# Optimization experiments

Measured on AMD Instinct MI355X. Metric: run time of the kernel, lower is better.

Reference implementation:

```python
import jax, jax.numpy as jnp
import numpy as np

DECAY = 0.99
EPSILON = 1e-05
CODEBOOK_SIZE = 1024
DIM = 128


def setup_inputs() -> dict:
    key = jax.random.key(0)
    k1, k2, k3, k4 = jax.random.split(key, 4)
    x = jax.random.normal(k1, (8, 8192, DIM), dtype=jnp.float32)
    embed = jax.random.normal(k2, (CODEBOOK_SIZE, DIM), dtype=jnp.float32)
    cluster_size = jax.random.uniform(k3, (CODEBOOK_SIZE,), dtype=jnp.float32)
    embed_avg = jax.random.normal(k4, (CODEBOOK_SIZE, DIM), dtype=jnp.float32)
    return {"x": x, "embed": embed, "cluster_size": cluster_size, "embed_avg": embed_avg}


def reference(x, embed, cluster_size, embed_avg):
    shape = x.shape
    flat = x.reshape(-1, shape[-1])  # [N, dim]

    # quantize: negative squared euclidean distance, argmax == nearest code
    dist = -(jnp.sum(flat * flat, axis=1, keepdims=True)
             - 2.0 * flat @ embed.T
             + jnp.sum(embed * embed, axis=1)[None, :])  # [N, K]
    embed_ind = jnp.argmax(dist, axis=-1)  # [N]

    quantize = embed[embed_ind].reshape(shape)            # dequantize
    embed_ind_out = embed_ind.reshape(shape[:-1])

    # training-time EMA updates (one-hot expressed as segment_sum)
    batch_cluster_size = jax.ops.segment_sum(
        jnp.ones_like(embed_ind, dtype=flat.dtype), embed_ind,
        num_segments=CODEBOOK_SIZE)                       # == one_hot.sum(0)
    new_cluster_size = cluster_size * DECAY + (1.0 - DECAY) * batch_cluster_size

    embed_sum = jax.ops.segment_sum(flat, embed_ind,
                                    num_segments=CODEBOOK_SIZE)  # == (x.T @ one_hot).T
    new_embed_avg = embed_avg * DECAY + (1.0 - DECAY) * embed_sum

    total = new_cluster_size.sum()
    smoothed = (new_cluster_size + EPSILON) / (total + CODEBOOK_SIZE * EPSILON)
    smoothed_counts = smoothed * total
    new_embed = new_embed_avg / smoothed_counts[:, None]

    return quantize, embed_ind_out, new_cluster_size, new_embed_avg, new_embed
```

## Files before the change

kernel.cpp:

```cpp
#include <hip/hip_runtime.h>
#include <math.h>

#define DIM 128
#define KCODES 1024
#define NROWS 65536

typedef short bf16x8 __attribute__((ext_vector_type(8)));
typedef float f32x4 __attribute__((ext_vector_type(4)));

#define WS_COUNTS 0
#define WS_ESUM   1024
#define WS_IOFF   132096
#define WS_TOTAL  133120
#define WS_ENORM2 133124
#define WS_EBF    134148
#define WS_WIN    461828
#define WS_SORTED 527364
#define WS_SCODE  592900

#define OFF_Q   0
#define OFF_IND 8388608
#define OFF_NCS 8454144
#define OFF_NEA 8455168
#define OFF_NE  8586240

static __device__ __forceinline__ unsigned short f2bf(float f) {
    unsigned u = __float_as_uint(f);
    unsigned r = (u + 0x7FFFu + ((u >> 16) & 1u)) >> 16;
    return (unsigned short)r;
}

static __device__ __forceinline__ void gload_lds16(const unsigned short* g,
                                                   unsigned short* l) {
    __builtin_amdgcn_global_load_lds(
        (const __attribute__((address_space(1))) void*)g,
        (__attribute__((address_space(3))) void*)l, 16, 0, 0);
}

__global__ __launch_bounds__(64) void k_prep(const float* __restrict__ embed,
                                             unsigned short* __restrict__ ebf,
                                             float* __restrict__ en2,
                                             float* __restrict__ counts,
                                             float* __restrict__ esum,
                                             int* __restrict__ cursor) {
    int k = blockIdx.x;
    int l = threadIdx.x;
    if (l == 0) { counts[k] = 0.0f; cursor[k] = 0; }
    *(float2*)&esum[(size_t)k * DIM + l * 2] = (float2){0.0f, 0.0f};
    float2 v = *(const float2*)&embed[(size_t)k * DIM + l * 2];
    ushort2 b;
    b.x = f2bf(v.x);
    b.y = f2bf(v.y);
    *(ushort2*)&ebf[(k * DIM + l * 2) ^ ((k & 7) << 3)] = b;
    float s = v.x * v.x + v.y * v.y;
    #pragma unroll
    for (int off = 32; off; off >>= 1) s += __shfl_xor(s, off);
    if (l == 0) en2[k] = 512.0f - 0.5f * s;
}

__global__ __launch_bounds__(512, 4) void k_fused(const float* __restrict__ x,
                                                  const float* __restrict__ embed,
                                                  const unsigned short* __restrict__ ebf,
                                                  const float* __restrict__ en2g,
                                                  int* __restrict__ win_g,
                                                  float* __restrict__ counts,
                                                  float* __restrict__ out) {
    __shared__ unsigned short buf[2][128 * 128];
    __shared__ float en2s[KCODES];
    __shared__ int winS[128];

    const int tid = threadIdx.x;
    const int row0 = blockIdx.x * 128;

    #pragma unroll
    for (int i = 0; i < 2; ++i) en2s[i * 512 + tid] = en2g[i * 512 + tid];

    #pragma unroll
    for (int i = 0; i < 8; ++i) {
        int idx4 = i * 512 + tid;
        int lin = idx4 * 4;
        int r = lin >> 7, d = lin & 127;
        float4 v = *(const float4*)&x[(size_t)(row0 + r) * DIM + d];
        ushort4 b;
        b.x = f2bf(v.x); b.y = f2bf(v.y); b.z = f2bf(v.z); b.w = f2bf(v.w);
        *(ushort4*)&buf[0][(r * 128 + d) ^ ((r & 7) << 3)] = b;
    }
    __syncthreads();

    const int lane = tid & 63;
    const int wv = tid >> 6;
    const int ch = wv & 1;
    const int rh = (wv >> 1) * 32;
    const int l15 = lane & 15;
    const int q = lane >> 4;
    const int swz = (l15 & 7) << 3;

    #pragma unroll
    for (int i = 0; i < 4; ++i) {
        int idx8 = i * 512 + tid;
        gload_lds16(&ebf[idx8 * 8], &buf[1][idx8 * 8]);
    }

    bf16x8 af[4][2];
    #pragma unroll
    for (int ks = 0; ks < 4; ++ks)
        #pragma unroll
        for (int t = 0; t < 2; ++t)
            af[ks][t] = *(const bf16x8*)&buf[0][((rh + t * 16 + l15) * 128 + ks * 32 + q * 8) ^ swz];
    __syncthreads();

    float m1[2][4], m2[2][4];
    #pragma unroll
    for (int a = 0; a < 2; ++a)
        #pragma unroll
        for (int b = 0; b < 4; ++b) { m1[a][b] = 0.0f; m2[a][b] = 0.0f; }

    for (int ct = 0; ct < 8; ++ct) {
        const int c0 = ct * 128;
        const unsigned short* cbuf = buf[1 ^ (ct & 1)];

        if (ct < 7) {
            unsigned short* nbuf = buf[ct & 1];
            const unsigned short* gsrc = ebf + (size_t)(c0 + 128) * DIM;
            #pragma unroll
            for (int i = 0; i < 4; ++i) {
                int idx8 = i * 512 + tid;
                gload_lds16(&gsrc[idx8 * 8], &nbuf[idx8 * 8]);
            }
        }

        f32x4 acc[2][4];
        #pragma unroll
        for (int cl = 0; cl < 4; ++cl) {
            float en = en2s[c0 + ch * 64 + cl * 16 + l15];
            #pragma unroll
            for (int rt = 0; rt < 2; ++rt) acc[rt][cl] = (f32x4){en, en, en, en};
        }

        __builtin_amdgcn_s_setprio(1);
        #pragma unroll
        for (int ks = 0; ks < 4; ++ks) {
            bf16x8 bfr[4];
            #pragma unroll
            for (int cl = 0; cl < 4; ++cl)
                bfr[cl] = *(const bf16x8*)&cbuf[((ch * 64 + cl * 16 + l15) * 128 + ks * 32 + q * 8) ^ swz];
            #pragma unroll
            for (int rt = 0; rt < 2; ++rt)
                #pragma unroll
                for (int cl = 0; cl < 4; ++cl)
                    acc[rt][cl] = __builtin_amdgcn_mfma_f32_16x16x32_bf16(af[ks][rt], bfr[cl],
                                                                          acc[rt][cl], 0, 0, 0);
        }

        #pragma unroll
        for (int cp = 0; cp < 2; ++cp) {
            unsigned cu0 = (unsigned)(c0 + ch * 64 + cp * 32 + l15);
            unsigned cu1 = cu0 + 16u;
            #pragma unroll
            for (int rt = 0; rt < 2; ++rt)
                #pragma unroll
                for (int rg = 0; rg < 4; ++rg) {
                    float sa = acc[rt][cp * 2][rg];
                    float sb = acc[rt][cp * 2 + 1][rg];
                    float a = __uint_as_float((__float_as_uint(sa) & ~1023u) | cu0);
                    float b = __uint_as_float((__float_as_uint(sb) & ~1023u) | cu1);
                    m2[rt][rg] = fmaxf(m2[rt][rg],
                                       __builtin_amdgcn_fmed3f(a, b, m1[rt][rg]));
                    m1[rt][rg] = fmaxf(fmaxf(a, b), m1[rt][rg]);
                }
        }
        __builtin_amdgcn_s_setprio(0);

        __syncthreads();
    }

    float* scratch = (float*)buf[0];
    unsigned* hist = (unsigned*)buf[0] + 512;

    #pragma unroll
    for (int rt = 0; rt < 2; ++rt)
        #pragma unroll
        for (int rg = 0; rg < 4; ++rg) {
            float a1 = m1[rt][rg], a2 = m2[rt][rg];
            #pragma unroll
            for (int off = 1; off <= 8; off <<= 1) {
                float o1 = __shfl_xor(a1, off);
                float o2 = __shfl_xor(a2, off);
                float t = fmaxf(a2, o2);
                a2 = __builtin_amdgcn_fmed3f(a1, o1, t);
                a1 = fmaxf(a1, o1);
            }
            if (l15 == 0) {
                int row = rh + rt * 16 + q * 4 + rg;
                scratch[row * 4 + ch * 2 + 0] = a1;
                scratch[row * 4 + ch * 2 + 1] = a2;
            }
        }

    #pragma unroll
    for (int i = 0; i < 2; ++i) hist[i * 512 + tid] = 0u;
    __syncthreads();

    {
        const int sub = tid & 15;
        const int g = tid >> 4;
        #pragma unroll 2
        for (int rr = 0; rr < 4; ++rr) {
            const int lrow = g * 4 + rr;
            const float* sp = &scratch[lrow * 4];
            int ci[4];
            ci[0] = (int)(__float_as_uint(sp[0]) & 1023u);
            ci[1] = (int)(__float_as_uint(sp[1]) & 1023u);
            ci[2] = (int)(__float_as_uint(sp[2]) & 1023u);
            ci[3] = (int)(__float_as_uint(sp[3]) & 1023u);

            const float* xr = &x[(size_t)(row0 + lrow) * DIM + sub * 4];
            float4 xa = *(const float4*)xr;
            float4 xb = *(const float4*)(xr + 64);

            double d[4];
            #pragma unroll
            for (int j = 0; j < 4; ++j) {
                const float* er2 = &embed[(size_t)ci[j] * DIM + sub * 4];
                float4 ea4 = *(const float4*)er2;
                float4 eb4 = *(const float4*)(er2 + 64);
                double t0 = (double)xa.x - (double)ea4.x;
                double t1 = (double)xa.y - (double)ea4.y;
                double t2 = (double)xa.z - (double)ea4.z;
                double t3 = (double)xa.w - (double)ea4.w;
                double t4 = (double)xb.x - (double)eb4.x;
                double t5 = (double)xb.y - (double)eb4.y;
                double t6 = (double)xb.z - (double)eb4.z;
                double t7 = (double)xb.w - (double)eb4.w;
                d[j] = ((t0 * t0 + t1 * t1) + (t2 * t2 + t3 * t3)) +
                       ((t4 * t4 + t5 * t5) + (t6 * t6 + t7 * t7));
            }
            #pragma unroll
            for (int off = 1; off <= 8; off <<= 1) {
                #pragma unroll
                for (int j = 0; j < 4; ++j) d[j] += __shfl_xor(d[j], off);
            }

            int win = ci[0];
            double dw = d[0];
            #pragma unroll
            for (int j = 1; j < 4; ++j) {
                bool b = (d[j] < dw) || (d[j] == dw && ci[j] < win);
                dw = b ? d[j] : dw;
                win = b ? ci[j] : win;
            }
            if (sub == 0) winS[lrow] = win;
        }
    }
    __syncthreads();

    if (tid < 128) {
        int w = winS[tid];
        atomicAdd(&hist[w], 1u);
        win_g[row0 + tid] = w;
        out[OFF_IND + row0 + tid] = (float)w;
    }

    #pragma unroll 4
    for (int i = 0; i < 16; ++i) {
        int lrow = wv * 16 + i;
        int w = winS[lrow];
        float2 v = *(const float2*)&embed[(size_t)w * DIM + lane * 2];
        *(float2*)&out[OFF_Q + (size_t)(row0 + lrow) * DIM + lane * 2] = v;
    }

    __syncthreads();
    #pragma unroll
    for (int i = 0; i < 2; ++i) {
        unsigned c = hist[i * 512 + tid];
        if (c) atomicAdd(&counts[i * 512 + tid], (float)c);
    }
}

__global__ __launch_bounds__(1024) void k_scansort(const float* __restrict__ cs,
                                                   const int* __restrict__ win_arr,
                                                   float* __restrict__ ws,
                                                   int* __restrict__ sorted,
                                                   int* __restrict__ scode,
                                                   float* __restrict__ out) {
    __shared__ int h[KCODES];
    __shared__ int bs[KCODES];
    __shared__ int wsum[16];
    __shared__ float wtot[16];
    const float* counts = ws + WS_COUNTS;
    int* cursor = (int*)(ws + WS_IOFF);

    const int t = threadIdx.x;
    h[t] = 0;
    __syncthreads();
    const int row = blockIdx.x * 1024 + t;
    const int w = win_arr[row];
    const int r = atomicAdd(&h[w], 1);

    const int lane = t & 63, wvi = t >> 6;
    const float cf = counts[t];
    const int c = (int)cf;
    int v = c;
    #pragma unroll
    for (int off = 1; off < 64; off <<= 1) {
        int o = __shfl_up(v, off);
        if (lane >= off) v += o;
    }
    if (lane == 63) wsum[wvi] = v;
    if (blockIdx.x == 0) {
        float ncs = cs[t] * 0.99f + 0.01f * cf;
        out[OFF_NCS + t] = ncs;
        float nf = ncs;
        #pragma unroll
        for (int off = 32; off; off >>= 1) nf += __shfl_xor(nf, off);
        if (lane == 0) wtot[wvi] = nf;
    }
    __syncthreads();

    int base = 0;
    for (int i = 0; i < wvi; ++i) base += wsum[i];
    const int gbase = base + v - c;

    if (blockIdx.x == 0 && t == 0) {
        float tt = 0.f;
        for (int i = 0; i < 16; ++i) tt += wtot[i];
        ws[WS_TOTAL] = tt;
    }

    const int cnt = h[t];
    if (cnt) bs[t] = gbase + atomicAdd(&cursor[t], cnt);
    __syncthreads();
    const int pos = bs[w] + r;
    sorted[pos] = row;
    scode[pos] = w;
}

__global__ __launch_bounds__(256) void k_segsum(const float* __restrict__ x,
                                                const int* __restrict__ sorted,
                                                const int* __restrict__ scode,
                                                float* __restrict__ esum) {
    const int lane = threadIdx.x & 63;
    const int wv = threadIdx.x >> 6;
    const int base = blockIdx.x * 256 + wv * 64;
    const int l15 = lane & 15;

    float ax = 0.f, ay = 0.f;
    int cur = -1;

    #pragma unroll
    for (int cc = 0; cc < 4; ++cc) {
        const int p = base + cc * 16 + l15;
        const int srow = sorted[p];
        const int sc = scode[p];
        if (cc == 0) cur = __shfl(sc, 0);
        #pragma unroll
        for (int j = 0; j < 16; ++j) {
            int row = __shfl(srow, j);
            int c = __shfl(sc, j);
            if (c != cur) {
                atomicAdd(&esum[cur * DIM + lane * 2], ax);
                atomicAdd(&esum[cur * DIM + lane * 2 + 1], ay);
                ax = 0.f; ay = 0.f;
                cur = c;
            }
            float2 v = *(const float2*)&x[(size_t)row * DIM + lane * 2];
            ax += v.x;
            ay += v.y;
        }
    }
    atomicAdd(&esum[cur * DIM + lane * 2], ax);
    atomicAdd(&esum[cur * DIM + lane * 2 + 1], ay);
}

__global__ __launch_bounds__(256) void k_embed(const float* __restrict__ ea,
                                               const float* __restrict__ ws,
                                               float* __restrict__ out) {
    int i = blockIdx.x * 256 + threadIdx.x;
    int k = i >> 7;
    float nea = ea[i] * 0.99f + 0.01f * ws[WS_ESUM + i];
    out[OFF_NEA + i] = nea;
    float total = ws[WS_TOTAL];
    float ncs = out[OFF_NCS + k];
    float sm = (ncs + 1e-5f) / (total + 1024.0f * 1e-5f);
    out[OFF_NE + i] = nea / (sm * total);
}

extern "C" void kernel_launch(void* const* d_in, const int* in_sizes, int n_in,
                              void* d_out, int out_size, void* d_ws, size_t ws_size,
                              hipStream_t stream) {
    const float* x     = (const float*)d_in[0];
    const float* embed = (const float*)d_in[1];
    const float* cs    = (const float*)d_in[2];
    const float* ea    = (const float*)d_in[3];
    float* out = (float*)d_out;
    float* ws  = (float*)d_ws;

    k_prep<<<KCODES, 64, 0, stream>>>(embed, (unsigned short*)(ws + WS_EBF),
                                      ws + WS_ENORM2, ws + WS_COUNTS, ws + WS_ESUM,
                                      (int*)(ws + WS_IOFF));
    k_fused<<<NROWS / 128, 512, 0, stream>>>(x, embed,
                                             (const unsigned short*)(ws + WS_EBF),
                                             ws + WS_ENORM2, (int*)(ws + WS_WIN),
                                             ws + WS_COUNTS, out);
    k_scansort<<<NROWS / 1024, 1024, 0, stream>>>(cs, (const int*)(ws + WS_WIN), ws,
                                                  (int*)(ws + WS_SORTED),
                                                  (int*)(ws + WS_SCODE), out);
    k_segsum<<<NROWS / 256, 256, 0, stream>>>(x, (const int*)(ws + WS_SORTED),
                                              (const int*)(ws + WS_SCODE), ws + WS_ESUM);
    k_embed<<<131072 / 256, 256, 0, stream>>>(ea, ws, out);
}
```

Measured before the change: 152.8 us.

## Fuse per-code segment sum into main kernel with block-local counting sort

Moves the embed_sum segment reduction into the fused distance/argmax kernel. Each 128-row block counting-sorts its winners in shared memory, then atomically adds per-code partial sums of x to the global accumulator. This removes the global scan/sort and segsum kernels, the win/sorted/scode workspace traffic, and a global re-read of x through indirection. In exchange the main kernel gets a longer tail, and the global atomics become more fragmented, since runs are only merged within a block of 128 rows.

```diff
diff --git a/kernel.cpp b/kernel.cpp
--- a/kernel.cpp
+++ b/kernel.cpp
@@ -10,13 +10,9 @@
 
 #define WS_COUNTS 0
 #define WS_ESUM   1024
-#define WS_IOFF   132096
 #define WS_TOTAL  133120
 #define WS_ENORM2 133124
 #define WS_EBF    134148
-#define WS_WIN    461828
-#define WS_SORTED 527364
-#define WS_SCODE  592900
 
 #define OFF_Q   0
 #define OFF_IND 8388608
@@ -41,11 +37,10 @@
                                              unsigned short* __restrict__ ebf,
                                              float* __restrict__ en2,
                                              float* __restrict__ counts,
-                                             float* __restrict__ esum,
-                                             int* __restrict__ cursor) {
+                                             float* __restrict__ esum) {
     int k = blockIdx.x;
     int l = threadIdx.x;
-    if (l == 0) { counts[k] = 0.0f; cursor[k] = 0; }
+    if (l == 0) counts[k] = 0.0f;
     *(float2*)&esum[(size_t)k * DIM + l * 2] = (float2){0.0f, 0.0f};
     float2 v = *(const float2*)&embed[(size_t)k * DIM + l * 2];
     ushort2 b;
@@ -62,12 +57,13 @@
                                                   const float* __restrict__ embed,
                                                   const unsigned short* __restrict__ ebf,
                                                   const float* __restrict__ en2g,
-                                                  int* __restrict__ win_g,
                                                   float* __restrict__ counts,
+                                                  float* __restrict__ esum,
                                                   float* __restrict__ out) {
     __shared__ unsigned short buf[2][128 * 128];
     __shared__ float en2s[KCODES];
     __shared__ int winS[128];
+    __shared__ int wsumS[8];
 
     const int tid = threadIdx.x;
     const int row0 = blockIdx.x * 128;
@@ -176,6 +172,8 @@
 
     float* scratch = (float*)buf[0];
     unsigned* hist = (unsigned*)buf[0] + 512;
+    unsigned* bbase = (unsigned*)buf[0] + 1536;
+    int* lorder = (int*)((unsigned*)buf[0] + 2560);
 
     #pragma unroll
     for (int rt = 0; rt < 2; ++rt)
@@ -254,11 +252,11 @@
     }
     __syncthreads();
 
+    int myw = 0, myr = 0;
     if (tid < 128) {
-        int w = winS[tid];
-        atomicAdd(&hist[w], 1u);
-        win_g[row0 + tid] = w;
-        out[OFF_IND + row0 + tid] = (float)w;
+        myw = winS[tid];
+        myr = (int)atomicAdd(&hist[myw], 1u);
+        out[OFF_IND + row0 + tid] = (float)myw;
     }
 
     #pragma unroll 4
@@ -268,108 +266,79 @@
         float2 v = *(const float2*)&embed[(size_t)w * DIM + lane * 2];
         *(float2*)&out[OFF_Q + (size_t)(row0 + lrow) * DIM + lane * 2] = v;
     }
-
-    __syncthreads();
-    #pragma unroll
-    for (int i = 0; i < 2; ++i) {
-        unsigned c = hist[i * 512 + tid];
-        if (c) atomicAdd(&counts[i * 512 + tid], (float)c);
-    }
-}
-
-__global__ __launch_bounds__(1024) void k_scansort(const float* __restrict__ cs,
-                                                   const int* __restrict__ win_arr,
-                                                   float* __restrict__ ws,
-                                                   int* __restrict__ sorted,
-                                                   int* __restrict__ scode,
-                                                   float* __restrict__ out) {
-    __shared__ int h[KCODES];
-    __shared__ int bs[KCODES];
-    __shared__ int wsum[16];
-    __shared__ float wtot[16];
-    const float* counts = ws + WS_COUNTS;
-    int* cursor = (int*)(ws + WS_IOFF);
-
-    const int t = threadIdx.x;
-    h[t] = 0;
-    __syncthreads();
-    const int row = blockIdx.x * 1024 + t;
-    const int w = win_arr[row];
-    const int r = atomicAdd(&h[w], 1);
-
-    const int lane = t & 63, wvi = t >> 6;
-    const float cf = counts[t];
-    const int c = (int)cf;
-    int v = c;
+    __syncthreads();
+
+    unsigned hc0 = hist[2 * tid], hc1 = hist[2 * tid + 1];
+    unsigned ps = hc0 + hc1;
+    unsigned v = ps;
     #pragma unroll
     for (int off = 1; off < 64; off <<= 1) {
-        int o = __shfl_up(v, off);
+        unsigned o = __shfl_up(v, off);
         if (lane >= off) v += o;
     }
-    if (lane == 63) wsum[wvi] = v;
-    if (blockIdx.x == 0) {
-        float ncs = cs[t] * 0.99f + 0.01f * cf;
-        out[OFF_NCS + t] = ncs;
-        float nf = ncs;
-        #pragma unroll
-        for (int off = 32; off; off >>= 1) nf += __shfl_xor(nf, off);
-        if (lane == 0) wtot[wvi] = nf;
-    }
-    __syncthreads();
-
-    int base = 0;
-    for (int i = 0; i < wvi; ++i) base += wsum[i];
-    const int gbase = base + v - c;
-
-    if (blockIdx.x == 0 && t == 0) {
-        float tt = 0.f;
-        for (int i = 0; i < 16; ++i) tt += wtot[i];
-        ws[WS_TOTAL] = tt;
-    }
-
-    const int cnt = h[t];
-    if (cnt) bs[t] = gbase + atomicAdd(&cursor[t], cnt);
-    __syncthreads();
-    const int pos = bs[w] + r;
-    sorted[pos] = row;
-    scode[pos] = w;
-}
-
-__global__ __launch_bounds__(256) void k_segsum(const float* __restrict__ x,
-                                                const int* __restrict__ sorted,
-                                                const int* __restrict__ scode,
-                                                float* __restrict__ esum) {
-    const int lane = threadIdx.x & 63;
-    const int wv = threadIdx.x >> 6;
-    const int base = blockIdx.x * 256 + wv * 64;
-    const int l15 = lane & 15;
-
-    float ax = 0.f, ay = 0.f;
-    int cur = -1;
-
-    #pragma unroll
-    for (int cc = 0; cc < 4; ++cc) {
-        const int p = base + cc * 16 + l15;
-        const int srow = sorted[p];
-        const int sc = scode[p];
-        if (cc == 0) cur = __shfl(sc, 0);
+    if (lane == 63) wsumS[wv] = (int)v;
+    __syncthreads();
+    unsigned wb = 0;
+    for (int i = 0; i < wv; ++i) wb += (unsigned)wsumS[i];
+    unsigned pb = wb + v - ps;
+    bbase[2 * tid] = pb;
+    bbase[2 * tid + 1] = pb + hc0;
+    __syncthreads();
+
+    if (tid < 128) lorder[bbase[myw] + (unsigned)myr] = tid;
+    __syncthreads();
+
+    {
+        const int p0 = wv * 16;
+        int lrow_p = lorder[p0 + l15];
+        int code_p = winS[lrow_p];
+        float ax = 0.f, ay = 0.f;
+        int cur = __shfl(code_p, 0);
         #pragma unroll
         for (int j = 0; j < 16; ++j) {
-            int row = __shfl(srow, j);
-            int c = __shfl(sc, j);
+            int lrow = __shfl(lrow_p, j);
+            int c = __shfl(code_p, j);
             if (c != cur) {
                 atomicAdd(&esum[cur * DIM + lane * 2], ax);
                 atomicAdd(&esum[cur * DIM + lane * 2 + 1], ay);
                 ax = 0.f; ay = 0.f;
                 cur = c;
             }
-            float2 v = *(const float2*)&x[(size_t)row * DIM + lane * 2];
-            ax += v.x;
-            ay += v.y;
-        }
-    }
-    atomicAdd(&esum[cur * DIM + lane * 2], ax);
-    atomicAdd(&esum[cur * DIM + lane * 2 + 1], ay);
+            float2 xv = *(const float2*)&x[(size_t)(row0 + lrow) * DIM + lane * 2];
+            ax += xv.x;
+            ay += xv.y;
+        }
+        atomicAdd(&esum[cur * DIM + lane * 2], ax);
+        atomicAdd(&esum[cur * DIM + lane * 2 + 1], ay);
+    }
+
+    #pragma unroll
+    for (int i = 0; i < 2; ++i) {
+        unsigned c = hist[i * 512 + tid];
+        if (c) atomicAdd(&counts[i * 512 + tid], (float)c);
+    }
+}
+
+__global__ __launch_bounds__(1024) void k_ncs(const float* __restrict__ cs,
+                                              float* __restrict__ out,
+                                              float* __restrict__ ws) {
+    __shared__ float wtot[16];
+    const float* counts = ws + WS_COUNTS;
+    int t = threadIdx.x;
+    int lane = t & 63, w = t >> 6;
+    float cf = counts[t];
+    float ncs = cs[t] * 0.99f + 0.01f * cf;
+    out[OFF_NCS + t] = ncs;
+    float nf = ncs;
+    #pragma unroll
+    for (int off = 32; off; off >>= 1) nf += __shfl_xor(nf, off);
+    if (lane == 0) wtot[w] = nf;
+    __syncthreads();
+    if (t == 0) {
+        float tt = 0.f;
+        for (int i = 0; i < 16; ++i) tt += wtot[i];
+        ws[WS_TOTAL] = tt;
+    }
 }
 
 __global__ __launch_bounds__(256) void k_embed(const float* __restrict__ ea,
@@ -396,16 +365,11 @@
     float* ws  = (float*)d_ws;
 
     k_prep<<<KCODES, 64, 0, stream>>>(embed, (unsigned short*)(ws + WS_EBF),
-                                      ws + WS_ENORM2, ws + WS_COUNTS, ws + WS_ESUM,
-                                      (int*)(ws + WS_IOFF));
+                                      ws + WS_ENORM2, ws + WS_COUNTS, ws + WS_ESUM);
     k_fused<<<NROWS / 128, 512, 0, stream>>>(x, embed,
                                              (const unsigned short*)(ws + WS_EBF),
-                                             ws + WS_ENORM2, (int*)(ws + WS_WIN),
-                                             ws + WS_COUNTS, out);
-    k_scansort<<<NROWS / 1024, 1024, 0, stream>>>(cs, (const int*)(ws + WS_WIN), ws,
-                                                  (int*)(ws + WS_SORTED),
-                                                  (int*)(ws + WS_SCODE), out);
-    k_segsum<<<NROWS / 256, 256, 0, stream>>>(x, (const int*)(ws + WS_SORTED),
-                                              (const int*)(ws + WS_SCODE), ws + WS_ESUM);
+                                             ws + WS_ENORM2, ws + WS_COUNTS,
+                                             ws + WS_ESUM, out);
+    k_ncs<<<1, 1024, 0, stream>>>(cs, out, ws);
     k_embed<<<131072 / 256, 256, 0, stream>>>(ea, ws, out);
 }
```

Measured after the change: 191.6 us. 1.25x slower.
